# Kernel optimization log

Measured on AMD Instinct MI355X. Metric: run time of the kernel, lower is better.

## Reference

```python
import jax, jax.numpy as jnp
import numpy as np

B, S, E, H = 8, 1024, 512, 8
NEG = -1e10


def setup_inputs() -> dict:
    key = jax.random.key(0)
    ks = jax.random.split(key, 8)
    k = jax.random.normal(ks[0], (B, S, E), dtype=jnp.float32)
    v = jax.random.normal(ks[1], (B, S, E), dtype=jnp.float32)
    q = jax.random.normal(ks[2], (B, S, E), dtype=jnp.float32)
    # causal mask, broadcastable like torch masked_fill
    mask = jnp.tril(jnp.ones((S, S), dtype=jnp.int32))[None, None]
    sc = 1.0 / np.sqrt(E)
    Wk = jax.random.normal(ks[3], (H * E, E), dtype=jnp.float32) * sc
    Wq = jax.random.normal(ks[4], (H * E, E), dtype=jnp.float32) * sc
    Wv = jax.random.normal(ks[5], (H * E, E), dtype=jnp.float32) * sc
    Wo = jax.random.normal(ks[6], (E, H * E), dtype=jnp.float32) * (1.0 / np.sqrt(H * E))
    bo = jnp.zeros((E,), dtype=jnp.float32)
    return {"k": k, "v": v, "q": q, "mask": mask,
            "Wk": Wk, "Wq": Wq, "Wv": Wv, "Wo": Wo, "bo": bo}


def reference(k, v, q, mask, Wk, Wq, Wv, Wo, bo):
    b, q_len, e = q.shape
    k_len, v_len = k.shape[1], v.shape[1]
    h = Wk.shape[0] // e
    scale = jnp.sqrt(jnp.asarray(e // h, dtype=jnp.float32))
    # projections E -> H*E (torch Linear: x @ W.T)
    wk = (k @ Wk.T).reshape(b, h, k_len, e)   # raw reshape, matches torch .view
    wq = (q @ Wq.T).reshape(b, h, q_len, e)
    wv = (v @ Wv.T).reshape(b, h, v_len, e)
    energy = jnp.einsum('bhqe,bhke->bhqk', wq, wk)
    energy = jnp.where(mask == 0, NEG, energy)  # mask applied BEFORE scaling, as in source
    energy = energy / scale
    attn = jax.nn.softmax(energy, axis=-1)
    f = jnp.einsum('bhqk,bhke->bhqe', attn, wv)
    f = jnp.transpose(f, (0, 2, 1, 3)).reshape(b, q_len, h * e)
    return f @ Wo.T + bo
```

## Files before the change

kernel.cpp:

```cpp
#include <hip/hip_runtime.h>


typedef _Float16 half8 __attribute__((ext_vector_type(8)));
typedef _Float16 half4v __attribute__((ext_vector_type(4)));
typedef float f32x4 __attribute__((ext_vector_type(4)));

typedef __attribute__((address_space(3))) unsigned int lds_u32_t;
typedef __attribute__((address_space(1))) unsigned int g_u32_t;

__device__ __forceinline__ void glds16(const void* g, void* l) {
  __builtin_amdgcn_global_load_lds((const g_u32_t*)g, (lds_u32_t*)l, 16, 0, 0);
}

template <int NT>
__device__ __forceinline__ void gemm128x256_core(const _Float16* __restrict__ A,
                                                 const _Float16* __restrict__ B,
                                                 int lda, int ldb,
                                                 _Float16* smem, f32x4 (&acc)[4][8]) {
  int tid = (int)threadIdx.x;
  int w = tid >> 6, lane = tid & 63;
  int wr2 = (w >> 1) * 32;
  int wc2 = (w & 1) * 64;
  int lr = lane & 15, hi = lane >> 4;
  int sp = ((((lane & 1) << 2) + hi) ^ ((lr >> 1) & 7)) << 3;
  int aBase = (wr2 + (lr >> 1)) * 64 + sp;
  int bBase = 4096 + (wc2 + (lr >> 1)) * 64 + sp;

  int srcA[2], srcB[4], dstA[2], dstB[4];
#pragma unroll
  for (int e = 0; e < 2; e++) {
    int X = e * 4096 + tid * 16;
    int rp = X >> 7;
    int s = ((X >> 4) & 7) ^ (rp & 7);
    srcA[e] = (2 * rp + (s >> 2)) * lda + ((s & 3) << 3);
    dstA[e] = e * 2048 + w * 512;
  }
#pragma unroll
  for (int e = 0; e < 4; e++) {
    int X = e * 4096 + tid * 16;
    int rp = X >> 7;
    int s = ((X >> 4) & 7) ^ (rp & 7);
    srcB[e] = (2 * rp + (s >> 2)) * ldb + ((s & 3) << 3);
    dstB[e] = 4096 + e * 2048 + w * 512;
  }

#pragma unroll
  for (int e = 0; e < 2; e++) glds16(A + srcA[e], smem + dstA[e]);
#pragma unroll
  for (int e = 0; e < 4; e++) glds16(B + srcB[e], smem + dstB[e]);
  if (NT > 1) {
#pragma unroll
    for (int e = 0; e < 2; e++) glds16(A + srcA[e] + 32, smem + 12288 + dstA[e]);
#pragma unroll
    for (int e = 0; e < 4; e++) glds16(B + srcB[e] + 32, smem + 12288 + dstB[e]);
  }

#pragma unroll
  for (int t = 0; t < NT; t++) {
    if (t + 1 < NT) asm volatile("s_waitcnt vmcnt(6)" ::: "memory");
    else            asm volatile("s_waitcnt vmcnt(0)" ::: "memory");
    __builtin_amdgcn_s_barrier();
    __builtin_amdgcn_sched_barrier(0);
    const _Float16* As = smem + (t % 3) * 12288;
    half8 a[4], b[4], c[4];
#pragma unroll
    for (int ni = 0; ni < 4; ni++) b[ni] = *(const half8*)&As[bBase + ni * 512];
#pragma unroll
    for (int mi = 0; mi < 4; mi++) a[mi] = *(const half8*)&As[aBase + mi * 512];
    if (t + 2 < NT) {
      _Float16* nb = smem + ((t + 2) % 3) * 12288;
#pragma unroll
      for (int e = 0; e < 2; e++) glds16(A + srcA[e] + (t + 2) * 32, nb + dstA[e]);
#pragma unroll
      for (int e = 0; e < 4; e++) glds16(B + srcB[e] + (t + 2) * 32, nb + dstB[e]);
    }
    __builtin_amdgcn_sched_barrier(0);
#pragma unroll
    for (int ni = 0; ni < 4; ni++)
      c[ni] = *(const half8*)&As[bBase + (ni + 4) * 512];
    __builtin_amdgcn_s_setprio(1);
#pragma unroll
    for (int mi = 0; mi < 4; mi++)
#pragma unroll
      for (int ni = 0; ni < 4; ni++)
        acc[mi][ni] = __builtin_amdgcn_mfma_f32_16x16x32_f16(a[mi], b[ni],
                                                             acc[mi][ni], 0, 0, 0);
#pragma unroll
    for (int mi = 0; mi < 4; mi++)
#pragma unroll
      for (int ni = 0; ni < 4; ni++)
        acc[mi][ni + 4] = __builtin_amdgcn_mfma_f32_16x16x32_f16(a[mi], c[ni],
                                                                 acc[mi][ni + 4], 0, 0, 0);
    __builtin_amdgcn_s_setprio(0);
    asm volatile("s_waitcnt lgkmcnt(0)" ::: "memory");
    __builtin_amdgcn_sched_barrier(0);
  }
  __syncthreads();
}

__device__ __forceinline__ void epilogue128x256(f32x4 (&acc)[4][8], _Float16* lds,
                                                _Float16* Cp, size_t cOff,
                                                int i0, int j0, int ldc) {
  int tid = (int)threadIdx.x;
  int w = tid >> 6, lane = tid & 63;
  int wr = (w >> 1) * 64, wc = (w & 1) * 128;
  int r0 = (lane >> 4) * 4, cl = lane & 15;
  _Float16* T = lds + w * 4096;
#pragma unroll
  for (int h = 0; h < 2; h++) {
#pragma unroll
    for (int mi = 0; mi < 4; mi++)
#pragma unroll
      for (int ni = 0; ni < 4; ni++) {
        int colb = ni * 16 + cl;
#pragma unroll
        for (int r = 0; r < 4; r++) {
          int row = mi * 16 + r0 + r;
          T[row * 64 + ((((colb >> 3) ^ row) & 7) << 3) + (colb & 7)] =
              (_Float16)acc[mi][h * 4 + ni][r];
        }
      }
#pragma unroll
    for (int st = 0; st < 8; st++) {
      int row = st * 8 + (lane >> 3);
      int c8 = lane & 7;
      half8 hh = *(const half8*)&T[row * 64 + (((c8 ^ row) & 7) << 3)];
      *(half8*)(Cp + cOff + (size_t)(i0 + wr + row) * ldc + j0 + wc + h * 64 + c8 * 8) = hh;
    }
  }
}

template <int HG>
__global__ __launch_bounds__(256, 2) void proj256(const _Float16* __restrict__ in16,
                                                  const _Float16* __restrict__ W16,
                                                  _Float16* __restrict__ Qp,
                                                  _Float16* __restrict__ Kp,
                                                  _Float16* __restrict__ Vp) {
  __shared__ __align__(16) _Float16 smem[36864];
  int x = (int)blockIdx.x, Y = (int)blockIdx.y;
  int work = (x & 7) * (HG * 16) + (x >> 3);
  int it = work >> 4, jt = work & 15;
  const _Float16* A = in16 + (size_t)Y * HG * 524288 + (size_t)it * 65536;
  const _Float16* B = W16 + (size_t)Y * 2097152 + (size_t)jt * 131072;
  _Float16* C = (Y == 0 ? Qp : (Y == 1 ? Kp : Vp));
  f32x4 acc[4][8] = {};
  gemm128x256_core<16>(A, B, 512, 512, smem, acc);
  epilogue128x256(acc, smem, C, 0, it * 128, jt * 256, 4096);
}

template <int HG>
__global__ __launch_bounds__(256, 2) void vwo256(const _Float16* __restrict__ Vp,
                                                 const _Float16* __restrict__ WoG,
                                                 _Float16* __restrict__ VWo) {
  __shared__ __align__(16) _Float16 smem[36864];
  int x = (int)blockIdx.x, Y = (int)blockIdx.y, Z = (int)blockIdx.z;
  size_t z = (size_t)Z * HG + Y;
  int i0 = (x >> 2) * 128, j0 = (x & 3) * 256;
  const _Float16* A = WoG + (size_t)Y * 512 + (size_t)i0 * 4096;
  const _Float16* B = Vp + z * 524288 + (size_t)j0 * 512;
  f32x4 acc[4][8] = {};
  gemm128x256_core<16>(A, B, 4096, 512, smem, acc);
  epilogue128x256(acc, smem, VWo, z * 524288, i0, j0, 1024);
}

template <int HG>
__global__ __launch_bounds__(256, 2) void energy256(const _Float16* __restrict__ Qp,
                                                    const _Float16* __restrict__ Kp,
                                                    _Float16* __restrict__ E) {
  __shared__ __align__(16) _Float16 smem[36864];
  int x = (int)blockIdx.x, Y = (int)blockIdx.y, Z = (int)blockIdx.z;
  size_t z = (size_t)Z * HG + Y;
  int ti, tj;
  if (x < 8)       { tj = 0; ti = x; }
  else if (x < 14) { tj = 1; ti = x - 6; }
  else if (x < 18) { tj = 2; ti = x - 10; }
  else             { tj = 3; ti = x - 12; }
  int i0 = ti * 128, j0 = tj * 256;
  const _Float16* A = Qp + z * 524288 + (size_t)i0 * 512;
  const _Float16* B = Kp + z * 524288 + (size_t)j0 * 512;
  f32x4 acc[4][8] = {};
  gemm128x256_core<16>(A, B, 512, 512, smem, acc);
  epilogue128x256(acc, smem, E, z * 1048576, i0, j0, 1024);
}

__device__ __forceinline__ void epilogue_atomic(f32x4 (&acc)[4][4], float* Cp,
                                                size_t cOff, int i0, int j0, int ldc) {
  int tid = (int)threadIdx.x;
  int w = tid >> 6, lane = tid & 63;
  int wr = (w >> 1) * 64, wc = (w & 1) * 64;
  int r0 = (lane >> 4) * 4, col = lane & 15;
#pragma unroll
  for (int mi = 0; mi < 4; mi++)
#pragma unroll
    for (int ni = 0; ni < 4; ni++)
#pragma unroll
      for (int r = 0; r < 4; r++)
        unsafeAtomicAdd(Cp + cOff + (size_t)(i0 + wr + mi * 16 + r0 + r) * ldc +
                            j0 + wc + ni * 16 + col,
                        acc[mi][ni][r]);
}

template <int HG, int HL>
__global__ __launch_bounds__(256, 2) void pv2(const _Float16* __restrict__ E,
                                              const _Float16* __restrict__ VWo,
                                              float* __restrict__ out) {
  __shared__ __align__(16) _Float16 smem[24576];
  int x = (int)blockIdx.x, Y = (int)blockIdx.y, Z = (int)blockIdx.z;
  int i0 = (x >> 2) * 128, j0 = (x & 3) * 128;
  size_t z0 = (size_t)Z * HG + (size_t)Y * HL;
  const _Float16* EA = E + z0 * 1048576 + (size_t)i0 * 1024;
  const _Float16* BB = VWo + z0 * 524288 + (size_t)j0 * 1024;

  int tid = (int)threadIdx.x;
  int w = tid >> 6, lane = tid & 63;
  int wr2 = (w >> 1) * 32;
  int wc2 = (w & 1) * 32;
  int lr = lane & 15, hi = lane >> 4;
  int sp = ((((lane & 1) << 2) + hi) ^ ((lr >> 1) & 7)) << 3;
  int aBase = (wr2 + (lr >> 1)) * 64 + sp;
  int bBase = 4096 + (wc2 + (lr >> 1)) * 64 + sp;

  int srcP[2], dstE_[2];
#pragma unroll
  for (int e = 0; e < 2; e++) {
    int X = e * 4096 + tid * 16;
    int rp = X >> 7;
    int s = ((X >> 4) & 7) ^ (rp & 7);
    srcP[e] = (2 * rp + (s >> 2)) * 1024 + ((s & 3) << 3);
    dstE_[e] = e * 2048 + w * 512;
  }

  int NTr = (i0 >> 5) + 4;
  int total = HL * NTr;

#pragma unroll
  for (int e = 0; e < 2; e++) glds16(EA + srcP[e], smem + dstE_[e]);
#pragma unroll
  for (int e = 0; e < 2; e++) glds16(BB + srcP[e], smem + 4096 + dstE_[e]);
#pragma unroll
  for (int e = 0; e < 2; e++) glds16(EA + srcP[e] + 32, smem + 8192 + dstE_[e]);
#pragma unroll
  for (int e = 0; e < 2; e++) glds16(BB + srcP[e] + 32, smem + 12288 + dstE_[e]);

  f32x4 acc[4][4] = {};
  int hs = 0, ts = 2;
  int bufc = 0, bufs = 2;
  for (int s = 0; s < total; s++) {
    if (s + 1 < total) asm volatile("s_waitcnt vmcnt(4)" ::: "memory");
    else               asm volatile("s_waitcnt vmcnt(0)" ::: "memory");
    __builtin_amdgcn_s_barrier();
    __builtin_amdgcn_sched_barrier(0);
    const _Float16* As = smem + bufc * 8192;
    half8 a[4], b[4];
#pragma unroll
    for (int ni = 0; ni < 4; ni++) b[ni] = *(const half8*)&As[bBase + ni * 512];
#pragma unroll
    for (int mi = 0; mi < 4; mi++) a[mi] = *(const half8*)&As[aBase + mi * 512];
    if (s + 2 < total) {
      const _Float16* Ah = EA + (size_t)hs * 1048576;
      const _Float16* Bh = BB + (size_t)hs * 524288;
      _Float16* nb = smem + bufs * 8192;
      int ko = ts * 32;
#pragma unroll
      for (int e = 0; e < 2; e++) glds16(Ah + srcP[e] + ko, nb + dstE_[e]);
#pragma unroll
      for (int e = 0; e < 2; e++) glds16(Bh + srcP[e] + ko, nb + 4096 + dstE_[e]);
      ts++; if (ts == NTr) { ts = 0; hs++; }
      bufs = (bufs == 2) ? 0 : bufs + 1;
    }
    __builtin_amdgcn_sched_barrier(0);
    __builtin_amdgcn_s_setprio(1);
#pragma unroll
    for (int mi = 0; mi < 4; mi++)
#pragma unroll
      for (int ni = 0; ni < 4; ni++)
        acc[mi][ni] = __builtin_amdgcn_mfma_f32_16x16x32_f16(a[mi], b[ni],
                                                             acc[mi][ni], 0, 0, 0);
    __builtin_amdgcn_s_setprio(0);
    asm volatile("s_waitcnt lgkmcnt(0)" ::: "memory");
    __builtin_amdgcn_sched_barrier(0);
    bufc = (bufc == 2) ? 0 : bufc + 1;
  }
  epilogue_atomic(acc, out, (size_t)Z * 524288, i0, j0, 512);
}

__global__ __launch_bounds__(256) void softmax_rows(void* __restrict__ Ep) {
  int R = (int)blockIdx.x * 4 + ((int)threadIdx.x >> 6);
  int lane = (int)threadIdx.x & 63;
  int i = R & 1023;
  int nt = (i >> 8) + 1;
  _Float16* row = (_Float16*)Ep + (size_t)R * 1024;
  float x[16];
  float m = -3.0e38f;
#pragma unroll
  for (int t = 0; t < 4; t++) {
    if (t < nt) {
      int j0 = t * 256 + lane * 4;
      half4v h = *(const half4v*)(row + j0);
#pragma unroll
      for (int c = 0; c < 4; c++) {
        float v = (j0 + c <= i) ? (float)h[c] * 0.125f : -3.0e38f;
        x[t * 4 + c] = v;
        m = fmaxf(m, v);
      }
    }
  }
#pragma unroll
  for (int s = 32; s > 0; s >>= 1) m = fmaxf(m, __shfl_xor(m, s, 64));
  float p[16];
  float sum = 0.0f;
#pragma unroll
  for (int t = 0; t < 4; t++) {
    if (t < nt) {
#pragma unroll
      for (int c = 0; c < 4; c++) {
        p[t * 4 + c] = exp2f((x[t * 4 + c] - m) * 1.44269504f);
        sum += p[t * 4 + c];
      }
    }
  }
#pragma unroll
  for (int s = 32; s > 0; s >>= 1) sum += __shfl_xor(sum, s, 64);
  float inv = 1.0f / sum;
#pragma unroll
  for (int t = 0; t < 4; t++) {
    if (t < nt) {
      int j0 = t * 256 + lane * 4;
      half4v h;
#pragma unroll
      for (int c = 0; c < 4; c++) h[c] = (_Float16)(p[t * 4 + c] * inv);
      *(half4v*)(row + j0) = h;
    }
  }
}

__global__ __launch_bounds__(256) void wbconv(const float* __restrict__ Wq,
                                              const float* __restrict__ Wk,
                                              const float* __restrict__ Wv,
                                              const float* __restrict__ Wo,
                                              _Float16* __restrict__ W16,
                                              float* __restrict__ out,
                                              const float* __restrict__ bo) {
  int bx = (int)blockIdx.x;
  if (bx < 4096) {
    size_t base = ((size_t)bx * 256 + threadIdx.x) * 8;
    int wid = (int)(base >> 21);
    size_t off = base & 2097151;
    const float* src = wid == 0 ? Wq : (wid == 1 ? Wk : (wid == 2 ? Wv : Wo));
    float4 a = *(const float4*)(src + off);
    float4 b = *(const float4*)(src + off + 4);
    half8 h;
    h[0] = (_Float16)a.x; h[1] = (_Float16)a.y; h[2] = (_Float16)a.z; h[3] = (_Float16)a.w;
    h[4] = (_Float16)b.x; h[5] = (_Float16)b.y; h[6] = (_Float16)b.z; h[7] = (_Float16)b.w;
    *(half8*)(W16 + base) = h;
  } else {
    size_t idx = ((size_t)(bx - 4096) * 256 + threadIdx.x) * 4;
    *(float4*)(out + idx) = *(const float4*)(bo + (idx & 511));
  }
}

template <int HG>
__global__ __launch_bounds__(256) void inconv(const float* __restrict__ q,
                                              const float* __restrict__ k,
                                              const float* __restrict__ v,
                                              _Float16* __restrict__ dst) {
  int Y = (int)blockIdx.y;
  size_t base = ((size_t)blockIdx.x * 256 + threadIdx.x) * 8;
  size_t b = base / (HG * 65536);
  size_t within = base - b * (HG * 65536);
  const float* src = (Y == 0 ? q : (Y == 1 ? k : v)) + b * 524288 + within;
  float4 a = ((const float4*)src)[0];
  float4 c = ((const float4*)src)[1];
  half8 h;
  h[0] = (_Float16)a.x; h[1] = (_Float16)a.y; h[2] = (_Float16)a.z; h[3] = (_Float16)a.w;
  h[4] = (_Float16)c.x; h[5] = (_Float16)c.y; h[6] = (_Float16)c.z; h[7] = (_Float16)c.w;
  *(half8*)(dst + (size_t)Y * HG * 524288 + base) = h;
}

template <int HG>
static void run_pipeline(const float* q_in, const float* k_in, const float* v_in,
                         const float* Wq, const float* Wk, const float* Wv,
                         const float* Wo, const float* bo, float* out, char* ws,
                         hipStream_t stream) {
  const int NG = 8 / HG;
  const long zc = 8 * HG;
  _Float16* W16 = (_Float16*)ws;
  _Float16* in16 = W16 + 8388608;
  _Float16* Qp = in16 + 3L * HG * 524288;
  _Float16* Kp = Qp + zc * 524288;
  _Float16* VWo = Kp + zc * 524288;
  _Float16* E = VWo + zc * 524288;
  _Float16* Vp = E;
  _Float16* Wo16 = W16 + 3 * 2097152;
  dim3 blk(256);

  wbconv<<<dim3(8192), blk, 0, stream>>>(Wq, Wk, Wv, Wo, W16, out, bo);

  constexpr int HL = (HG >= 2) ? 2 : 1;
  constexpr int YS = HG / HL;

  for (int g = 0; g < NG; g++) {
    inconv<HG><<<dim3(HG * 256, 3), blk, 0, stream>>>(
        q_in + (size_t)g * HG * 65536, k_in + (size_t)g * HG * 65536,
        v_in + (size_t)g * HG * 65536, in16);

    proj256<HG><<<dim3(HG * 128, 3), blk, 0, stream>>>(in16, W16, Qp, Kp, Vp);

    vwo256<HG><<<dim3(16, HG, 8), blk, 0, stream>>>(
        Vp, Wo16 + (size_t)g * HG * 512, VWo);

    energy256<HG><<<dim3(20, HG, 8), blk, 0, stream>>>(Qp, Kp, E);

    softmax_rows<<<dim3(zc * 256), blk, 0, stream>>>(E);

    pv2<HG, HL><<<dim3(32, YS, 8), blk, 0, stream>>>(E, VWo, out);
  }
}

extern "C" void kernel_launch(void* const* d_in, const int* in_sizes, int n_in,
                              void* d_out, int out_size, void* d_ws, size_t ws_size,
                              hipStream_t stream) {
  const float* k_in = (const float*)d_in[0];
  const float* v_in = (const float*)d_in[1];
  const float* q_in = (const float*)d_in[2];
  const float* Wk = (const float*)d_in[4];
  const float* Wq = (const float*)d_in[5];
  const float* Wv = (const float*)d_in[6];
  const float* Wo = (const float*)d_in[7];
  const float* bo = (const float*)d_in[8];
  float* out = (float*)d_out;
  char* ws = (char*)d_ws;

  if (ws_size >= (size_t)197132288)
    run_pipeline<4>(q_in, k_in, v_in, Wq, Wk, Wv, Wo, bo, out, ws, stream);
  else if (ws_size >= (size_t)106954752)
    run_pipeline<2>(q_in, k_in, v_in, Wq, Wk, Wv, Wo, bo, out, ws, stream);
  else
    run_pipeline<1>(q_in, k_in, v_in, Wq, Wk, Wv, Wo, bo, out, ws, stream);
}
```

Measured before the change: 539.2 us.

## Replace projection GEMM with 256x256 8-wave kernel using phased load/MFMA interleave

The QKV projection kernel moves from 128x256 tiles on 256-thread blocks to 256x256 tiles on 512-thread blocks. The new core double-buffers LDS and splits each K-step into four phases, each staging one quarter of the next tile with global_load_lds while running a 4x4 MFMA block under raised priority. Larger tiles raise arithmetic intensity and cut redundant global loads. In exchange it uses 128KB of LDS per block for one block per CU, has a smaller grid with fewer waves to hide latency, and adds many more barriers.

Measured after the change: 546.9 us. Within noise of the previous version (+1.4%).

```diff
diff --git a/kernel.cpp b/kernel.cpp
--- a/kernel.cpp
+++ b/kernel.cpp
@@ -10,6 +10,186 @@
 
 __device__ __forceinline__ void glds16(const void* g, void* l) {
   __builtin_amdgcn_global_load_lds((const g_u32_t*)g, (lds_u32_t*)l, 16, 0, 0);
+}
+
+template <int NT>
+__device__ __forceinline__ void gemm256_8ph(const _Float16* __restrict__ A,
+                                            const _Float16* __restrict__ B,
+                                            int lda, int ldb,
+                                            _Float16* smem, f32x4 (&acc)[8][4]) {
+  int tid = (int)threadIdx.x;
+  int w = tid >> 6, lane = tid & 63;
+  int wr = (w >> 2) * 128, wc = (w & 3) * 64;
+  int lr = lane & 15, hi = lane >> 4;
+  int sw0 = ((hi ^ (lr & 7)) << 3);
+  int sw1 = (((4 + hi) ^ (lr & 7)) << 3);
+  int aR = (wr + lr) * 64;
+  int bR = 16384 + (wc + lr) * 64;
+
+  int offA[2], offB[2], dstOff[2];
+#pragma unroll
+  for (int e = 0; e < 2; e++) {
+    int X = e * 8192 + tid * 16;
+    int r = X >> 7;
+    int s = (X >> 4) & 7;
+    offA[e] = r * lda + ((s ^ (r & 7)) << 3);
+    offB[e] = r * ldb + ((s ^ (r & 7)) << 3);
+    dstOff[e] = e * 4096 + w * 512;
+  }
+
+#define STAGE_HALF(t_, ht_, bufp_)                                             \
+  do {                                                                         \
+    if ((ht_) == 0) {                                                          \
+      glds16(A + offA[0] + (t_) * 64, (bufp_) + dstOff[0]);                    \
+      glds16(A + offA[1] + (t_) * 64, (bufp_) + dstOff[1]);                    \
+    } else if ((ht_) == 1) {                                                   \
+      glds16(B + offB[0] + (t_) * 64, (bufp_) + 16384 + dstOff[0]);            \
+      glds16(B + offB[1] + (t_) * 64, (bufp_) + 16384 + dstOff[1]);            \
+    } else if ((ht_) == 2) {                                                   \
+      glds16(A + 128 * lda + offA[0] + (t_) * 64, (bufp_) + 8192 + dstOff[0]); \
+      glds16(A + 128 * lda + offA[1] + (t_) * 64, (bufp_) + 8192 + dstOff[1]); \
+    } else {                                                                   \
+      glds16(B + 128 * ldb + offB[0] + (t_) * 64, (bufp_) + 24576 + dstOff[0]);\
+      glds16(B + 128 * ldb + offB[1] + (t_) * 64, (bufp_) + 24576 + dstOff[1]);\
+    }                                                                          \
+  } while (0)
+
+  STAGE_HALF(0, 0, smem); STAGE_HALF(0, 1, smem);
+  STAGE_HALF(0, 2, smem); STAGE_HALF(0, 3, smem);
+  asm volatile("s_waitcnt vmcnt(0)" ::: "memory");
+  __builtin_amdgcn_s_barrier();
+
+#pragma unroll
+  for (int t = 0; t < NT; t++) {
+    const _Float16* Bf = smem + (t & 1) * 32768;
+    _Float16* Nb = smem + ((t + 1) & 1) * 32768;
+    half8 a[4], b[4];
+#pragma unroll
+    for (int ni = 0; ni < 4; ni++) b[ni] = *(const half8*)&Bf[bR + ni * 1024 + sw0];
+#pragma unroll
+    for (int mi = 0; mi < 4; mi++) a[mi] = *(const half8*)&Bf[aR + mi * 1024 + sw0];
+    if (t + 1 < NT) STAGE_HALF(t + 1, 0, Nb);
+    __builtin_amdgcn_sched_barrier(0);
+    __builtin_amdgcn_s_barrier();
+    asm volatile("s_waitcnt lgkmcnt(0)" ::: "memory");
+    __builtin_amdgcn_sched_barrier(0);
+    __builtin_amdgcn_s_setprio(1);
+#pragma unroll
+    for (int mi = 0; mi < 4; mi++)
+#pragma unroll
+      for (int ni = 0; ni < 4; ni++)
+        acc[mi][ni] = __builtin_amdgcn_mfma_f32_16x16x32_f16(a[mi], b[ni],
+                                                             acc[mi][ni], 0, 0, 0);
+    __builtin_amdgcn_s_setprio(0);
+    __builtin_amdgcn_sched_barrier(0);
+    __builtin_amdgcn_s_barrier();
+#pragma unroll
+    for (int mi = 0; mi < 4; mi++) a[mi] = *(const half8*)&Bf[aR + (mi + 4) * 1024 + sw0];
+    if (t + 1 < NT) STAGE_HALF(t + 1, 1, Nb);
+    __builtin_amdgcn_sched_barrier(0);
+    __builtin_amdgcn_s_barrier();
+    asm volatile("s_waitcnt lgkmcnt(0)" ::: "memory");
+    __builtin_amdgcn_sched_barrier(0);
+    __builtin_amdgcn_s_setprio(1);
+#pragma unroll
+    for (int mi = 0; mi < 4; mi++)
+#pragma unroll
+      for (int ni = 0; ni < 4; ni++)
+        acc[mi + 4][ni] = __builtin_amdgcn_mfma_f32_16x16x32_f16(a[mi], b[ni],
+                                                                 acc[mi + 4][ni], 0, 0, 0);
+    __builtin_amdgcn_s_setprio(0);
+    __builtin_amdgcn_sched_barrier(0);
+    __builtin_amdgcn_s_barrier();
+#pragma unroll
+    for (int ni = 0; ni < 4; ni++) b[ni] = *(const half8*)&Bf[bR + ni * 1024 + sw1];
+#pragma unroll
+    for (int mi = 0; mi < 4; mi++) a[mi] = *(const half8*)&Bf[aR + mi * 1024 + sw1];
+    if (t + 1 < NT) STAGE_HALF(t + 1, 2, Nb);
+    __builtin_amdgcn_sched_barrier(0);
+    __builtin_amdgcn_s_barrier();
+    asm volatile("s_waitcnt lgkmcnt(0)" ::: "memory");
+    __builtin_amdgcn_sched_barrier(0);
+    __builtin_amdgcn_s_setprio(1);
+#pragma unroll
+    for (int mi = 0; mi < 4; mi++)
+#pragma unroll
+      for (int ni = 0; ni < 4; ni++)
+        acc[mi][ni] = __builtin_amdgcn_mfma_f32_16x16x32_f16(a[mi], b[ni],
+                                                             acc[mi][ni], 0, 0, 0);
+    __builtin_amdgcn_s_setprio(0);
+    __builtin_amdgcn_sched_barrier(0);
+    __builtin_amdgcn_s_barrier();
+#pragma unroll
+    for (int mi = 0; mi < 4; mi++) a[mi] = *(const half8*)&Bf[aR + (mi + 4) * 1024 + sw1];
+    if (t + 1 < NT) STAGE_HALF(t + 1, 3, Nb);
+    __builtin_amdgcn_sched_barrier(0);
+    __builtin_amdgcn_s_barrier();
+    asm volatile("s_waitcnt lgkmcnt(0)" ::: "memory");
+    __builtin_amdgcn_sched_barrier(0);
+    __builtin_amdgcn_s_setprio(1);
+#pragma unroll
+    for (int mi = 0; mi < 4; mi++)
+#pragma unroll
+      for (int ni = 0; ni < 4; ni++)
+        acc[mi + 4][ni] = __builtin_amdgcn_mfma_f32_16x16x32_f16(a[mi], b[ni],
+                                                                 acc[mi + 4][ni], 0, 0, 0);
+    __builtin_amdgcn_s_setprio(0);
+    __builtin_amdgcn_sched_barrier(0);
+    asm volatile("s_waitcnt vmcnt(0)" ::: "memory");
+    __builtin_amdgcn_s_barrier();
+  }
+#undef STAGE_HALF
+  __syncthreads();
+}
+
+__device__ __forceinline__ void epilogue256(f32x4 (&acc)[8][4], _Float16* lds,
+                                            _Float16* Cp, size_t cOff,
+                                            int i0, int j0, int ldc) {
+  int tid = (int)threadIdx.x;
+  int w = tid >> 6, lane = tid & 63;
+  int wr = (w >> 2) * 128, wc = (w & 3) * 64;
+  int r0 = (lane >> 4) * 4, cl = lane & 15;
+  _Float16* T = lds + w * 4096;
+#pragma unroll
+  for (int h = 0; h < 2; h++) {
+#pragma unroll
+    for (int mi = 0; mi < 4; mi++)
+#pragma unroll
+      for (int ni = 0; ni < 4; ni++) {
+        int colb = ni * 16 + cl;
+#pragma unroll
+        for (int r = 0; r < 4; r++) {
+          int row = mi * 16 + r0 + r;
+          T[row * 64 + ((((colb >> 3) ^ row) & 7) << 3) + (colb & 7)] =
+              (_Float16)acc[h * 4 + mi][ni][r];
+        }
+      }
+#pragma unroll
+    for (int st = 0; st < 8; st++) {
+      int row = st * 8 + (lane >> 3);
+      int c8 = lane & 7;
+      half8 hh = *(const half8*)&T[row * 64 + (((c8 ^ row) & 7) << 3)];
+      *(half8*)(Cp + cOff + (size_t)(i0 + wr + h * 64 + row) * ldc + j0 + wc + c8 * 8) = hh;
+    }
+  }
+}
+
+template <int HG>
+__global__ __launch_bounds__(512, 1) void proj8ph(const _Float16* __restrict__ in16,
+                                                  const _Float16* __restrict__ W16,
+                                                  _Float16* __restrict__ Qp,
+                                                  _Float16* __restrict__ Kp,
+                                                  _Float16* __restrict__ Vp) {
+  __shared__ __align__(16) _Float16 smem[65536];
+  int x = (int)blockIdx.x, Y = (int)blockIdx.y;
+  int work = (x & 7) * (HG * 8) + (x >> 3);
+  int it = work >> 4, jt = work & 15;
+  const _Float16* A = in16 + (size_t)Y * HG * 524288 + (size_t)it * 131072;
+  const _Float16* B = W16 + (size_t)Y * 2097152 + (size_t)jt * 131072;
+  _Float16* C = (Y == 0 ? Qp : (Y == 1 ? Kp : Vp));
+  f32x4 acc[8][4] = {};
+  gemm256_8ph<8>(A, B, 512, 512, smem, acc);
+  epilogue256(acc, smem, C, 0, it * 256, jt * 256, 4096);
 }
 
 template <int NT>
@@ -128,24 +308,6 @@
       *(half8*)(Cp + cOff + (size_t)(i0 + wr + row) * ldc + j0 + wc + h * 64 + c8 * 8) = hh;
     }
   }
-}
-
-template <int HG>
-__global__ __launch_bounds__(256, 2) void proj256(const _Float16* __restrict__ in16,
-                                                  const _Float16* __restrict__ W16,
-                                                  _Float16* __restrict__ Qp,
-                                                  _Float16* __restrict__ Kp,
-                                                  _Float16* __restrict__ Vp) {
-  __shared__ __align__(16) _Float16 smem[36864];
-  int x = (int)blockIdx.x, Y = (int)blockIdx.y;
-  int work = (x & 7) * (HG * 16) + (x >> 3);
-  int it = work >> 4, jt = work & 15;
-  const _Float16* A = in16 + (size_t)Y * HG * 524288 + (size_t)it * 65536;
-  const _Float16* B = W16 + (size_t)Y * 2097152 + (size_t)jt * 131072;
-  _Float16* C = (Y == 0 ? Qp : (Y == 1 ? Kp : Vp));
-  f32x4 acc[4][8] = {};
-  gemm128x256_core<16>(A, B, 512, 512, smem, acc);
-  epilogue128x256(acc, smem, C, 0, it * 128, jt * 256, 4096);
 }
 
 template <int HG>
@@ -393,6 +555,7 @@
   _Float16* Vp = E;
   _Float16* Wo16 = W16 + 3 * 2097152;
   dim3 blk(256);
+  dim3 blk5(512);
 
   wbconv<<<dim3(8192), blk, 0, stream>>>(Wq, Wk, Wv, Wo, W16, out, bo);
 
@@ -404,7 +567,7 @@
         q_in + (size_t)g * HG * 65536, k_in + (size_t)g * HG * 65536,
         v_in + (size_t)g * HG * 65536, in16);
 
-    proj256<HG><<<dim3(HG * 128, 3), blk, 0, stream>>>(in16, W16, Qp, Kp, Vp);
+    proj8ph<HG><<<dim3(HG * 64, 3), blk5, 0, stream>>>(in16, W16, Qp, Kp, Vp);
 
     vwo256<HG><<<dim3(16, HG, 8), blk, 0, stream>>>(
         Vp, Wo16 + (size_t)g * HG * 512, VWo);
```
